# Kernel optimization log

Hardware: AMD Instinct MI355X
Metric: run time of the kernel (lower is better)

The kernel has to match this reference:

```python
import jax, jax.numpy as jnp
import numpy as np

B = 1024      # batch
D_NUM = 100   # numeric features
N_CAT = 20    # categorical features
CARD = 100    # cardinality per categorical feature
D = 1024      # d_token
DH = 675      # int(d_token * 0.66)
NT = D_NUM + 1 + N_CAT  # 121 tokens (CLS + numeric + categorical)
E = 4         # num_experts
K = 2         # top_k
MID = 512     # ResidualHead mid dim = max(D//2, 16)
RH = 256      # router/alpha hidden = max(D//4, 16)


def _ln(x, g, b):
    m = x.mean(-1, keepdims=True)
    v = ((x - m) ** 2).mean(-1, keepdims=True)
    return (x - m) * jax.lax.rsqrt(v + 1e-5) * g + b


def setup_inputs() -> dict:
    key = jax.random.key(0)
    ks = jax.random.split(key, 20)

    def n(i, shape, s=0.02):
        return jax.random.normal(ks[i], shape, dtype=jnp.float32) * s

    return dict(
        x_num=jax.random.normal(ks[0], (B, D_NUM), dtype=jnp.float32),
        x_cat=jax.random.randint(ks[1], (B, N_CAT), 0, CARD),
        tok_w=n(2, (D_NUM + 1, D), 0.05),
        tok_b=n(3, (D_NUM + N_CAT, D), 0.05),
        cat_emb=n(4, (N_CAT * CARD, D), 0.05),
        ln_g=jnp.ones((D,), jnp.float32), ln_b=jnp.zeros((D,), jnp.float32),
        lin0_w=n(5, (D, 2 * DH)), lin0_b=jnp.zeros((2 * DH,), jnp.float32),
        sgu_ln_g=jnp.ones((DH,), jnp.float32), sgu_ln_b=jnp.zeros((DH,), jnp.float32),
        sgu_w=n(6, (NT, NT), 0.05), sgu_b=jnp.zeros((NT,), jnp.float32),
        lin1_w=n(7, (DH, D)), lin1_b=jnp.zeros((D,), jnp.float32),
        r_w1=n(8, (D, RH)), r_b1=jnp.zeros((RH,), jnp.float32),
        r_w2=n(9, (RH, E)), r_b2=jnp.zeros((E,), jnp.float32),
        a_w1=n(10, (D, RH)), a_b1=jnp.zeros((RH,), jnp.float32),
        a_w2=n(11, (RH, 1)), a_b2=jnp.full((1,), -4.0, jnp.float32),
        base_w=n(12, (D, 1)), base_b=jnp.zeros((1,), jnp.float32),
        gh_w1=n(13, (D, MID), 0.001), gh_b1=jnp.zeros((MID,), jnp.float32),
        gh_w2=n(14, (MID, 1), 0.001), gh_b2=jnp.zeros((1,), jnp.float32),
        ex_w1=n(15, (E, D, MID), 0.001), ex_b1=jnp.zeros((E, MID), jnp.float32),
        ex_w2=n(16, (E, MID), 0.001), ex_b2=jnp.zeros((E,), jnp.float32),
    )


def reference(x_num, x_cat, tok_w, tok_b, cat_emb, ln_g, ln_b, lin0_w, lin0_b,
              sgu_ln_g, sgu_ln_b, sgu_w, sgu_b, lin1_w, lin1_b,
              r_w1, r_b1, r_w2, r_b2, a_w1, a_b1, a_w2, a_b2,
              base_w, base_b, gh_w1, gh_b1, gh_w2, gh_b2,
              ex_w1, ex_b1, ex_w2, ex_b2):
    # ---- Tokenizer ----
    offsets = jnp.arange(N_CAT) * CARD
    xn = jnp.concatenate([jnp.ones((x_num.shape[0], 1), x_num.dtype), x_num], axis=1)  # [B, D_NUM+1]
    x = tok_w[None] * xn[:, :, None]                                  # [B, D_NUM+1, D]
    x = jnp.concatenate([x, cat_emb[x_cat + offsets[None]]], axis=1)  # [B, NT, D]
    bias_full = jnp.concatenate([jnp.zeros((1, D), tok_b.dtype), tok_b], axis=0)
    x = x + bias_full[None]
    # ---- gMLP layer (n_layers=1) ----
    xr = x
    h = _ln(x, ln_g, ln_b)
    h = jax.nn.gelu(h @ lin0_w + lin0_b, approximate=False)           # [B, NT, 2*DH]
    u, v = h[..., :DH], h[..., DH:]
    v = _ln(v, sgu_ln_g, sgu_ln_b)
    # SGU token-mixing: out[b,s,d] = sum_t v[b,t,d] * W[s,t] + bias[s]
    v = jnp.einsum('btd,st->bsd', v, sgu_w) + sgu_b[None, :, None]
    x = (u * v) @ lin1_w + lin1_b
    x = x + xr
    # ---- pooled hidden (CLS token) ----
    hidden = jax.nn.gelu(_ln(x[:, 0], ln_g, ln_b), approximate=False)  # [B, D]
    # ---- router + top-k sparsification ----
    logits = jax.nn.relu(hidden @ r_w1 + r_b1) @ r_w2 + r_b2           # [B, E]
    dense = jax.nn.softmax(logits, axis=-1)
    vals, idx = jax.lax.top_k(dense, K)
    sparse = jnp.zeros_like(dense).at[jnp.arange(dense.shape[0])[:, None], idx].set(vals)
    rw = sparse / jnp.clip(sparse.sum(-1, keepdims=True), 1e-8)
    # ---- local experts (small residual heads, vectorized over E) ----
    eh = jax.nn.relu(jnp.einsum('bd,edm->bem', hidden, ex_w1) + ex_b1[None])
    eo = jnp.einsum('bem,em->be', eh, ex_w2) + ex_b2[None]             # [B, E]
    local = (rw * eo).sum(-1, keepdims=True)                           # [B, 1]
    # ---- global residual, alpha gate, base head ----
    glob = jax.nn.relu(hidden @ gh_w1 + gh_b1) @ gh_w2 + gh_b2
    alpha = jax.nn.sigmoid(jax.nn.relu(hidden @ a_w1 + a_b1) @ a_w2 + a_b2)
    y_base = hidden @ base_w + base_b
    return y_base + alpha * (glob + local)                             # [B, 1]
```

## Files before the change

kernel.cpp:

```cpp
#include <hip/hip_runtime.h>
#include <math.h>

#define B_SZ 1024

typedef __attribute__((ext_vector_type(8))) short bf16x8;
typedef __attribute__((ext_vector_type(4))) float f32x4;
typedef __attribute__((ext_vector_type(4))) float floatx4;
typedef __attribute__((ext_vector_type(4))) unsigned short ushortx4;

#define GLOAD16(src, dst) __builtin_amdgcn_global_load_lds( \
    (const __attribute__((address_space(1))) void*)(src), \
    (__attribute__((address_space(3))) void*)(dst), 16, 0, 0)

__device__ __forceinline__ unsigned short f2bf(float f) {
  unsigned int u = __float_as_uint(f);
  u += 0x7fff + ((u >> 16) & 1);
  return (unsigned short)(u >> 16);
}
__device__ __forceinline__ float bf2f(unsigned short b) {
  return __uint_as_float(((unsigned int)b) << 16);
}
__device__ __forceinline__ floatx4 b4f(ushortx4 u) {
  floatx4 r;
  r[0] = bf2f(u[0]); r[1] = bf2f(u[1]); r[2] = bf2f(u[2]); r[3] = bf2f(u[3]);
  return r;
}
__device__ __forceinline__ float gelu_exact(float x) {
  return 0.5f * x * (1.0f + erff(x * 0.70710678118654752f));
}
__device__ __forceinline__ float gelu_fast(float x) {
  const float c0 = 2.3022586f;
  const float c1 = 0.10295465f;
  float z = x * __builtin_fmaf(x * x, c1, c0);
  float e = __builtin_amdgcn_exp2f(z);
  float r = __builtin_amdgcn_rcpf(e + 1.0f);
  return __builtin_fmaf(-x, r, x);
}
__device__ __forceinline__ float wred(float v) {
#pragma unroll
  for (int o = 32; o > 0; o >>= 1) v += __shfl_xor(v, o, 64);
  return v;
}

struct PrepArgs {
  const float* src[9];
  unsigned short* dst[9];
  int ldin[9]; int coff[9]; int Nsrc[9]; int Ksrc[9]; int Kp[9];
  int nbx[9]; int blk0[10];
};

__global__ __launch_bounds__(256)
void prep_all(PrepArgs J,
              const float* __restrict__ tok_w, const float* __restrict__ tok_b,
              const float* __restrict__ cat_emb,
              const float* __restrict__ ln_g, const float* __restrict__ ln_b,
              const float* __restrict__ r_b1, const float* __restrict__ a_b1,
              const float* __restrict__ gh_b1, const float* __restrict__ ex_b1,
              unsigned short* __restrict__ Amat,
              float* __restrict__ nstat, float* __restrict__ cstat,
              float* __restrict__ bcat)
{
  const int bid = blockIdx.x;
  const int tid = threadIdx.x;
  const int lane = tid & 63;
  const int NT = J.blk0[9];
  if (bid < NT) {
    __shared__ float tile[64][65];
    int j = 0;
    while (bid >= J.blk0[j + 1]) ++j;
    const int bx = bid - J.blk0[j];
    const int k0 = (bx % J.nbx[j]) * 64;
    const int n0 = (bx / J.nbx[j]) * 64;
    const float* in = J.src[j];
    unsigned short* out = J.dst[j];
    const int ldin = J.ldin[j], coff = J.coff[j], Nsrc = J.Nsrc[j], Ksrc = J.Ksrc[j], Kp = J.Kp[j];
    const int kx = tid & 63;
    const int ry = tid >> 6;
    for (int r = ry; r < 64; r += 4) {
      const int k = k0 + r;
      const int n = n0 + kx;
      tile[r][kx] = (k < Ksrc && n < Nsrc) ? in[(size_t)k * ldin + coff + n] : 0.f;
    }
    __syncthreads();
    for (int r = ry; r < 64; r += 4) {
      const int n = n0 + r;
      const int k = k0 + kx;
      out[(size_t)n * Kp + k] = f2bf(tile[kx][r]);
    }
  } else if (bid < NT + 576) {
    const int r = (bid - NT) * 4 + (tid >> 6);
    if (r >= 2304) return;
    unsigned short* out = Amat + (size_t)r * 1024;
    for (int k = lane * 4; k < 1024; k += 256) {
      floatx4 g = *(const floatx4*)(ln_g + k);
      floatx4 v;
      if (r <= 100) {
        floatx4 a = *(const floatx4*)(tok_w + (size_t)r * 1024 + k);
#pragma unroll
        for (int q = 0; q < 4; q++) v[q] = a[q] * g[q];
      } else if (r <= 200) {
        floatx4 a = *(const floatx4*)(tok_b + (size_t)(r - 101) * 1024 + k);
#pragma unroll
        for (int q = 0; q < 4; q++) v[q] = a[q] * g[q];
      } else if (r <= 2200) {
        const int j = r - 201;
        const int c = j / 100;
        floatx4 a = *(const floatx4*)(cat_emb + (size_t)j * 1024 + k);
        floatx4 bq = *(const floatx4*)(tok_b + (size_t)(100 + c) * 1024 + k);
#pragma unroll
        for (int q = 0; q < 4; q++) v[q] = (a[q] + bq[q]) * g[q];
      } else if (r == 2201) {
        v = g;
      } else if (r == 2202) {
        v = *(const floatx4*)(ln_b + k);
      } else {
        v[0] = 0.f; v[1] = 0.f; v[2] = 0.f; v[3] = 0.f;
      }
      ushortx4 o;
#pragma unroll
      for (int q = 0; q < 4; q++) o[q] = f2bf(v[q]);
      *(ushortx4*)(out + k) = o;
    }
  } else if (bid < NT + 576 + 526) {
    const int w = (bid - NT - 576) * 4 + (tid >> 6);
    if (w >= 2101) return;
    if (w <= 100) {
      const int t = w;
      const float* wr = tok_w + (size_t)t * 1024;
      const float* br = (t >= 1) ? (tok_b + (size_t)(t - 1) * 1024) : nullptr;
      float sw = 0, sww = 0, sb = 0, sbb = 0, swb = 0;
      for (int k = lane * 4; k < 1024; k += 256) {
        floatx4 a = *(const floatx4*)(wr + k);
#pragma unroll
        for (int q = 0; q < 4; q++) { sw += a[q]; sww += a[q] * a[q]; }
        if (br) {
          floatx4 bq = *(const floatx4*)(br + k);
#pragma unroll
          for (int q = 0; q < 4; q++) { sb += bq[q]; sbb += bq[q] * bq[q]; swb += a[q] * bq[q]; }
        }
      }
      sw = wred(sw); sww = wred(sww); sb = wred(sb); sbb = wred(sbb); swb = wred(swb);
      if (lane == 0) {
        float* ns = nstat + (size_t)t * 5;
        ns[0] = sw; ns[1] = sww; ns[2] = sb; ns[3] = sbb; ns[4] = swb;
      }
    } else {
      const int j = w - 101;
      const int c = j / 100;
      const float* ar = cat_emb + (size_t)j * 1024;
      const float* br = tok_b + (size_t)(100 + c) * 1024;
      float s1 = 0, s2 = 0;
      for (int k = lane * 4; k < 1024; k += 256) {
        floatx4 a = *(const floatx4*)(ar + k);
        floatx4 bq = *(const floatx4*)(br + k);
#pragma unroll
        for (int q = 0; q < 4; q++) { const float v = a[q] + bq[q]; s1 += v; s2 += v * v; }
      }
      s1 = wred(s1); s2 = wred(s2);
      if (lane == 0) { cstat[(size_t)j * 2] = s1; cstat[(size_t)j * 2 + 1] = s2; }
    }
  } else {
    const int n = (bid - NT - 1102) * 256 + tid;
    if (n >= 3072) return;
    float v;
    if (n < 256) v = r_b1[n];
    else if (n < 512) v = a_b1[n - 256];
    else if (n < 1024) v = gh_b1[n - 512];
    else v = ex_b1[n - 1024];
    bcat[n] = v;
  }
}

template<int EPI>
__device__ __forceinline__
void gemm64_body(int bid, const unsigned short* __restrict__ A, long pitchA,
                 const unsigned short* __restrict__ Bw, int K,
                 const float* __restrict__ bias, const float* __restrict__ extra,
                 int NB, int Nvalid, int ldo,
                 float* __restrict__ outf, unsigned short* __restrict__ outb)
{
  __shared__ unsigned short As[64 * 32];
  __shared__ unsigned short Bs[64 * 32];
  const int tid = threadIdx.x, lane = tid & 63, wv = tid >> 6;
  const int nb = bid % NB, mb = bid / NB;
  const int m0 = mb * 64, n0 = nb * 64;
  const int wr = (wv >> 1) << 5, wc = (wv & 1) << 5;
  const int fr = lane & 15, fq = lane >> 4;

  const unsigned short* srcA = A + (size_t)(m0 + (tid >> 2)) * pitchA + ((tid & 3) << 3);
  const unsigned short* srcB = Bw + (size_t)(n0 + (tid >> 2)) * K + ((tid & 3) << 3);

  f32x4 acc[2][2] = {};
  for (int k0 = 0; k0 < K; k0 += 32) {
    __syncthreads();
    GLOAD16(srcA + k0, &As[tid * 8]);
    GLOAD16(srcB + k0, &Bs[tid * 8]);
    __syncthreads();
    bf16x8 af[2], bw_[2];
#pragma unroll
    for (int i = 0; i < 2; i++) {
      af[i]  = *(const bf16x8*)&As[(wr + i * 16 + fr) * 32 + fq * 8];
      bw_[i] = *(const bf16x8*)&Bs[(wc + i * 16 + fr) * 32 + fq * 8];
    }
#pragma unroll
    for (int i = 0; i < 2; i++)
#pragma unroll
      for (int j = 0; j < 2; j++)
        acc[i][j] = __builtin_amdgcn_mfma_f32_16x16x32_bf16(af[i], bw_[j], acc[i][j], 0, 0, 0);
  }

#pragma unroll
  for (int i = 0; i < 2; i++)
#pragma unroll
    for (int j = 0; j < 2; j++) {
      const int n = n0 + wc + j * 16 + fr;
      if (n >= ldo) continue;
      const bool valid = (n < Nvalid);
      const float bv = (EPI == 3 || EPI == 4) ? 0.f : (valid ? bias[n] : 0.f);
      const float ev = (EPI == 0) ? extra[n] : 0.f;
#pragma unroll
      for (int q = 0; q < 4; q++) {
        const int m = m0 + wr + i * 16 + fq * 4 + q;
        const float a = acc[i][j][q];
        if (EPI == 0) {
          outf[(size_t)m * ldo + n] = a + bv + ev;
        } else if (EPI == 1) {
          outb[(size_t)m * ldo + n] = f2bf(fmaxf(a + bv, 0.f));
        } else if (EPI == 3) {
          outf[(size_t)m * ldo + n] = a;
        } else {
          outb[(size_t)m * ldo + n] = f2bf(a);
        }
      }
    }
}

template<int EPI>
__global__ __launch_bounds__(256)
void gemm64(const unsigned short* __restrict__ A, long pitchA,
            const unsigned short* __restrict__ Bw, int K,
            const float* __restrict__ bias, const float* __restrict__ extra,
            int NB, int Nvalid, int ldo,
            float* __restrict__ outf, unsigned short* __restrict__ outb)
{
  gemm64_body<EPI>(blockIdx.x, A, pitchA, Bw, K, bias, extra, NB, Nvalid, ldo, outf, outb);
}

__device__ __forceinline__
void ucon_body(int bid, const float* __restrict__ lin0_w, const float* __restrict__ nstat,
               const float* __restrict__ tok_w, const float* __restrict__ ln_g,
               const float* __restrict__ ln_b, const float* __restrict__ lin0_b,
               float* __restrict__ ucon)
{
  __shared__ float xk[1024];
  __shared__ float part[4][64];
  const int tid = threadIdx.x;
  const float m = nstat[0] * (1.f / 1024.f);
  const float ex2 = nstat[1] * (1.f / 1024.f);
  const float rs = rsqrtf(ex2 - m * m + 1e-5f);
  for (int k = tid; k < 1024; k += 256)
    xk[k] = bf2f(f2bf((tok_w[k] - m) * rs * ln_g[k] + ln_b[k]));
  __syncthreads();
  const int c = bid * 64 + (tid & 63);
  const int ks = tid >> 6;
  float acc = 0.f;
  for (int k = ks * 256; k < ks * 256 + 256; k++)
    acc = __builtin_fmaf(xk[k], bf2f(f2bf(lin0_w[(size_t)k * 1350 + c])), acc);
  part[ks][tid & 63] = acc;
  __syncthreads();
  if (tid < 64) {
    const int cc = bid * 64 + tid;
    if (cc < 704) {
      const float s = part[0][tid] + part[1][tid] + part[2][tid] + part[3][tid];
      ucon[cc] = (cc < 675) ? gelu_exact(s + lin0_b[cc]) : 0.f;
    }
  }
}

__global__ __launch_bounds__(256)
void tab_and_u(const unsigned short* __restrict__ Amat, const unsigned short* __restrict__ w0v,
               unsigned short* __restrict__ TABb,
               const float* __restrict__ lin0_w, const float* __restrict__ nstat,
               const float* __restrict__ tok_w, const float* __restrict__ ln_g,
               const float* __restrict__ ln_b, const float* __restrict__ lin0_b,
               float* __restrict__ ucon)
{
  if (blockIdx.x < 432)
    gemm64_body<4>(blockIdx.x, Amat, 1024, w0v, 1024, nullptr, nullptr, 12, 768, 768, nullptr, TABb);
  else
    ucon_body(blockIdx.x - 432, lin0_w, nstat, tok_w, ln_g, ln_b, lin0_b, ucon);
}

__global__ __launch_bounds__(256)
void cat_rows(const unsigned short* __restrict__ TABb, const float* __restrict__ nstat,
              const float* __restrict__ cstat, const float* __restrict__ lin0_b,
              unsigned short* __restrict__ catvalb, float* __restrict__ catsc)
{
  const int r = blockIdx.x * 4 + (threadIdx.x >> 6);
  const int lane = threadIdx.x & 63;
  if (r >= 2001) return;
  float m, ex2;
  const unsigned short* T1;
  if (r < 2000) {
    m = cstat[(size_t)r * 2] * (1.f / 1024.f);
    ex2 = cstat[(size_t)r * 2 + 1] * (1.f / 1024.f);
    T1 = TABb + (size_t)(201 + r) * 768;
  } else {
    m = nstat[0] * (1.f / 1024.f);
    ex2 = nstat[1] * (1.f / 1024.f);
    T1 = TABb;
  }
  const float rs = rsqrtf(ex2 - m * m + 1e-5f);
  const float ga = -m * rs;
  const unsigned short* R = TABb + (size_t)2201 * 768;
  const unsigned short* C = TABb + (size_t)2202 * 768;
  const int dl = lane << 2;
  float s = 0.f, ss = 0.f;
  unsigned short* outp = catvalb + (size_t)r * 768;
#pragma unroll
  for (int ch = 0; ch < 3; ch++) {
    const int d = ch * 256 + dl;
    floatx4 t1 = b4f(*(const ushortx4*)(T1 + d));
    floatx4 rr = b4f(*(const ushortx4*)(R + d));
    floatx4 cc = b4f(*(const ushortx4*)(C + d));
    ushortx4 o;
#pragma unroll
    for (int q = 0; q < 4; q++) {
      const int dd = d + q;
      const float c2 = (dd < 675) ? (cc[q] + lin0_b[675 + dd]) : 0.f;
      const float pre = __builtin_fmaf(rs, t1[q], __builtin_fmaf(ga, rr[q], c2));
      const float g = (dd < 675) ? gelu_fast(pre) : 0.f;
      o[q] = f2bf(g); s += g; ss = __builtin_fmaf(g, g, ss);
    }
    *(ushortx4*)(outp + d) = o;
  }
  s = wred(s); ss = wred(ss);
  const float mu = s * (1.f / 675.f);
  const float rho = rsqrtf(ss * (1.f / 675.f) - mu * mu + 1e-5f);
  if (lane == 0) { catsc[(size_t)r * 2] = mu; catsc[(size_t)r * 2 + 1] = rho; }
}

__global__ __launch_bounds__(512)
void fused_v2(const unsigned short* __restrict__ TABb, const float* __restrict__ nstat,
              const float* __restrict__ catsc, const unsigned short* __restrict__ catvalb,
              const float* __restrict__ x_num, const int* __restrict__ x_cat,
              const float* __restrict__ sgu_ln_g, const float* __restrict__ sgu_ln_b,
              const float* __restrict__ sgu_w, const float* __restrict__ sgu_b,
              const float* __restrict__ lin0_b, const float* __restrict__ ucon,
              unsigned short* __restrict__ uv)
{
  const int b0 = blockIdx.x, b1 = blockIdx.x + 512;
  const int tid = threadIdx.x, lane = tid & 63, wv = tid >> 6;
  __shared__ float Rls[768], Cls[768];
  __shared__ float alf[2][100], bet[2][100], gam[2][100], swt[100];
  __shared__ float wrc[2][21], catkb[2][21];
  __shared__ int catrowS[2][21];
  __shared__ float accw[8][768];
  __shared__ float kbw[2][8];
  __shared__ float wss_s;

  for (int d = tid; d < 768; d += 512) {
    Rls[d] = (d < 675) ? bf2f(TABb[(size_t)2201 * 768 + d]) : 0.f;
    Cls[d] = (d < 675) ? (bf2f(TABb[(size_t)2202 * 768 + d]) + lin0_b[675 + d]) : 0.f;
  }
  if (tid < 200) {
    const int bb = tid / 100, tt = tid % 100;
    const int b = bb ? b1 : b0;
    const float sc = x_num[b * 100 + tt];
    const float* ns = nstat + (size_t)(tt + 1) * 5;
    const float m = (sc * ns[0] + ns[2]) * (1.f / 1024.f);
    const float ex2 = (sc * sc * ns[1] + 2.f * sc * ns[4] + ns[3]) * (1.f / 1024.f);
    const float rs = rsqrtf(ex2 - m * m + 1e-5f);
    alf[bb][tt] = rs * sc; bet[bb][tt] = rs; gam[bb][tt] = -m * rs;
    if (bb == 0) swt[tt] = sgu_w[tt + 1];
  } else if (tid < 242) {
    const int idx = tid - 200;
    const int bb = idx / 21, ii = idx % 21;
    const int b = bb ? b1 : b0;
    int row; float sw;
    if (ii < 20) { row = x_cat[b * 20 + ii] + 100 * ii; sw = sgu_w[101 + ii]; }
    else { row = 2000; sw = sgu_w[0]; }
    const float mu = catsc[(size_t)row * 2], rho = catsc[(size_t)row * 2 + 1];
    const float wr = sw * rho;
    wrc[bb][ii] = wr; catkb[bb][ii] = wr * mu; catrowS[bb][ii] = row;
  } else if (tid >= 256 && tid < 320) {
    float s = (lane < 121 ? sgu_w[lane] : 0.f) + (lane + 64 < 121 ? sgu_w[lane + 64] : 0.f);
    s = wred(s);
    if (lane == 0) wss_s = s;
  }
  __syncthreads();

  float accA[12] = {}, accB[12] = {};
  float kbA = 0.f, kbB = 0.f;
  const int dl = lane << 2;

  for (int i = 0; i < 13; i++) {
    const int tt = wv + 8 * i;
    if (tt >= 100) break;
    const float a0 = alf[0][tt], be0 = bet[0][tt], ga0 = gam[0][tt];
    const float a1 = alf[1][tt], be1 = bet[1][tt], ga1 = gam[1][tt];
    const unsigned short* T1 = TABb + (size_t)(tt + 1) * 768;
    const unsigned short* T2 = TABb + (size_t)(101 + tt) * 768;
    float s0 = 0.f, ss0 = 0.f, s1 = 0.f, ss1 = 0.f;
    float va[12], vb[12];
#pragma unroll
    for (int ch = 0; ch < 3; ch++) {
      const int d = ch * 256 + dl;
      floatx4 t1 = b4f(*(const ushortx4*)(T1 + d));
      floatx4 t2 = b4f(*(const ushortx4*)(T2 + d));
      floatx4 rr = *(const floatx4*)(&Rls[d]);
      floatx4 cc = *(const floatx4*)(&Cls[d]);
#pragma unroll
      for (int q = 0; q < 4; q++) {
        const float pre0 = __builtin_fmaf(a0, t1[q], __builtin_fmaf(be0, t2[q], __builtin_fmaf(ga0, rr[q], cc[q])));
        const float g0 = gelu_fast(pre0);
        va[ch * 4 + q] = g0; s0 += g0; ss0 = __builtin_fmaf(g0, g0, ss0);
        const float pre1 = __builtin_fmaf(a1, t1[q], __builtin_fmaf(be1, t2[q], __builtin_fmaf(ga1, rr[q], cc[q])));
        const float g1 = gelu_fast(pre1);
        vb[ch * 4 + q] = g1; s1 += g1; ss1 = __builtin_fmaf(g1, g1, ss1);
      }
    }
    s0 = wred(s0); ss0 = wred(ss0); s1 = wred(s1); ss1 = wred(ss1);
    const float sw = swt[tt];
    const float mu0 = s0 * (1.f / 675.f);
    const float rho0 = rsqrtf(ss0 * (1.f / 675.f) - mu0 * mu0 + 1e-5f);
    const float w0 = sw * rho0;
    const float mu1 = s1 * (1.f / 675.f);
    const float rho1 = rsqrtf(ss1 * (1.f / 675.f) - mu1 * mu1 + 1e-5f);
    const float w1 = sw * rho1;
#pragma unroll
    for (int q = 0; q < 12; q++) {
      accA[q] = __builtin_fmaf(w0, va[q], accA[q]);
      accB[q] = __builtin_fmaf(w1, vb[q], accB[q]);
    }
    kbA = __builtin_fmaf(w0, mu0, kbA);
    kbB = __builtin_fmaf(w1, mu1, kbB);
  }

  for (int i = 0; i < 3; i++) {
    const int ii = wv + 8 * i;
    if (ii >= 21) break;
    {
      const float wr = wrc[0][ii];
      const unsigned short* cv = catvalb + (size_t)catrowS[0][ii] * 768;
#pragma unroll
      for (int ch = 0; ch < 3; ch++) {
        floatx4 v = b4f(*(const ushortx4*)(cv + ch * 256 + dl));
#pragma unroll
        for (int q = 0; q < 4; q++) accA[ch * 4 + q] = __builtin_fmaf(wr, v[q], accA[ch * 4 + q]);
      }
    }
    {
      const float wr = wrc[1][ii];
      const unsigned short* cv = catvalb + (size_t)catrowS[1][ii] * 768;
#pragma unroll
      for (int ch = 0; ch < 3; ch++) {
        floatx4 v = b4f(*(const ushortx4*)(cv + ch * 256 + dl));
#pragma unroll
        for (int q = 0; q < 4; q++) accB[ch * 4 + q] = __builtin_fmaf(wr, v[q], accB[ch * 4 + q]);
      }
    }
  }
  if (lane == 0) { kbw[0][wv] = kbA; kbw[1][wv] = kbB; }

  const float sb0 = sgu_b[0];

#pragma unroll
  for (int ch = 0; ch < 3; ch++)
    *(floatx4*)&accw[wv][ch * 256 + dl] = *(const floatx4*)&accA[ch * 4];
  __syncthreads();
  {
    float kbs = 0.f;
#pragma unroll
    for (int w = 0; w < 8; w++) kbs += kbw[0][w];
#pragma unroll
    for (int i = 0; i < 21; i++) kbs += catkb[0][i];
    const float wss = wss_s;
    for (int d = tid; d < 704; d += 512) {
      unsigned short o = 0;
      if (d < 675) {
        float a = 0.f;
#pragma unroll
        for (int w = 0; w < 8; w++) a += accw[w][d];
        const float v0 = sgu_ln_g[d] * (a - kbs) + sgu_ln_b[d] * wss + sb0;
        o = f2bf(ucon[d] * v0);
      }
      uv[(size_t)b0 * 704 + d] = o;
    }
  }
  __syncthreads();
#pragma unroll
  for (int ch = 0; ch < 3; ch++)
    *(floatx4*)&accw[wv][ch * 256 + dl] = *(const floatx4*)&accB[ch * 4];
  __syncthreads();
  {
    float kbs = 0.f;
#pragma unroll
    for (int w = 0; w < 8; w++) kbs += kbw[1][w];
#pragma unroll
    for (int i = 0; i < 21; i++) kbs += catkb[1][i];
    const float wss = wss_s;
    for (int d = tid; d < 704; d += 512) {
      unsigned short o = 0;
      if (d < 675) {
        float a = 0.f;
#pragma unroll
        for (int w = 0; w < 8; w++) a += accw[w][d];
        const float v0 = sgu_ln_g[d] * (a - kbs) + sgu_ln_b[d] * wss + sb0;
        o = f2bf(ucon[d] * v0);
      }
      uv[(size_t)b1 * 704 + d] = o;
    }
  }
}

__global__ __launch_bounds__(256)
void ln_gelu_hidden(const float* __restrict__ xfin,
                    const float* __restrict__ ln_g, const float* __restrict__ ln_b,
                    const float* __restrict__ base_w,
                    unsigned short* __restrict__ hid_bf, float* __restrict__ base_y)
{
  const int w = (blockIdx.x * 256 + threadIdx.x) >> 6;
  const int lane = threadIdx.x & 63;
  if (w >= B_SZ) return;
  const float* row = xfin + (size_t)w * 1024;
  float s = 0.f, ss = 0.f;
  for (int k = lane; k < 1024; k += 64) { float v = row[k]; s += v; ss += v * v; }
  s = wred(s); ss = wred(ss);
  const float m = s * (1.f / 1024.f);
  const float var = ss * (1.f / 1024.f) - m * m;
  const float rs = rsqrtf(var + 1e-5f);
  float bacc = 0.f;
  for (int k = lane; k < 1024; k += 64) {
    float v = gelu_fast((row[k] - m) * rs * ln_g[k] + ln_b[k]);
    hid_bf[(size_t)w * 1024 + k] = f2bf(v);
    bacc = __builtin_fmaf(v, base_w[k], bacc);
  }
  bacc = wred(bacc);
  if (lane == 0) base_y[w] = bacc;
}

__global__ __launch_bounds__(256)
void final_head(const unsigned short* __restrict__ H1, const float* __restrict__ base_y,
                const float* __restrict__ r_w2, const float* __restrict__ r_b2,
                const float* __restrict__ a_w2, const float* __restrict__ a_b2,
                const float* __restrict__ gh_w2, const float* __restrict__ gh_b2,
                const float* __restrict__ ex_w2, const float* __restrict__ ex_b2,
                const float* __restrict__ base_b,
                float* __restrict__ out)
{
  const int b = blockIdx.x;
  const int tid = threadIdx.x;
  const unsigned short* h1 = H1 + (size_t)b * 3072;
  float p[10];
#pragma unroll
  for (int i = 0; i < 10; i++) p[i] = 0.f;
  {
    const int m = tid;
    const float hr = bf2f(h1[m]);
    p[0] = hr * r_w2[m * 4 + 0];
    p[1] = hr * r_w2[m * 4 + 1];
    p[2] = hr * r_w2[m * 4 + 2];
    p[3] = hr * r_w2[m * 4 + 3];
    const float ha = bf2f(h1[256 + m]);
    p[4] = ha * a_w2[m];
  }
  for (int m = tid; m < 512; m += 256) {
    p[5] += bf2f(h1[512 + m]) * gh_w2[m];
#pragma unroll
    for (int e = 0; e < 4; e++)
      p[6 + e] += bf2f(h1[1024 + e * 512 + m]) * ex_w2[e * 512 + m];
  }

  __shared__ float red[10][4];
  const int lane = tid & 63, wv = tid >> 6;
#pragma unroll
  for (int i = 0; i < 10; i++) {
    const float v = wred(p[i]);
    if (lane == 0) red[i][wv] = v;
  }
  __syncthreads();
  if (tid == 0) {
    float s[10];
#pragma unroll
    for (int i = 0; i < 10; i++) s[i] = red[i][0] + red[i][1] + red[i][2] + red[i][3];
    float lg[4];
#pragma unroll
    for (int e = 0; e < 4; e++) lg[e] = s[e] + r_b2[e];
    const float mx = fmaxf(fmaxf(lg[0], lg[1]), fmaxf(lg[2], lg[3]));
    float den[4]; float dsum = 0.f;
#pragma unroll
    for (int e = 0; e < 4; e++) { den[e] = expf(lg[e] - mx); dsum += den[e]; }
#pragma unroll
    for (int e = 0; e < 4; e++) den[e] /= dsum;
    int i1 = 0;
    for (int e = 1; e < 4; e++) if (den[e] > den[i1]) i1 = e;
    int i2 = -1;
    for (int e = 0; e < 4; e++) { if (e == i1) continue; if (i2 < 0 || den[e] > den[i2]) i2 = e; }
    float eo[4];
#pragma unroll
    for (int e = 0; e < 4; e++) eo[e] = s[6 + e] + ex_b2[e];
    const float v1 = den[i1], v2 = den[i2];
    const float ssum = fmaxf(v1 + v2, 1e-8f);
    const float local = (v1 * eo[i1] + v2 * eo[i2]) / ssum;
    const float glob = s[5] + gh_b2[0];
    const float alpha = 1.0f / (1.0f + expf(-(s[4] + a_b2[0])));
    out[b] = base_y[b] + base_b[0] + alpha * (glob + local);
  }
}

extern "C" void kernel_launch(void* const* d_in, const int* in_sizes, int n_in,
                              void* d_out, int out_size, void* d_ws, size_t ws_size,
                              hipStream_t stream)
{
  const float* x_num  = (const float*)d_in[0];
  const int*   x_cat  = (const int*)d_in[1];
  const float* tok_w  = (const float*)d_in[2];
  const float* tok_b  = (const float*)d_in[3];
  const float* cat_emb= (const float*)d_in[4];
  const float* ln_g   = (const float*)d_in[5];
  const float* ln_b   = (const float*)d_in[6];
  const float* lin0_w = (const float*)d_in[7];
  const float* lin0_b = (const float*)d_in[8];
  const float* sgu_ln_g = (const float*)d_in[9];
  const float* sgu_ln_b = (const float*)d_in[10];
  const float* sgu_w  = (const float*)d_in[11];
  const float* sgu_b  = (const float*)d_in[12];
  const float* lin1_w = (const float*)d_in[13];
  const float* lin1_b = (const float*)d_in[14];
  const float* r_w1   = (const float*)d_in[15];
  const float* r_b1   = (const float*)d_in[16];
  const float* r_w2   = (const float*)d_in[17];
  const float* r_b2   = (const float*)d_in[18];
  const float* a_w1   = (const float*)d_in[19];
  const float* a_b1   = (const float*)d_in[20];
  const float* a_w2   = (const float*)d_in[21];
  const float* a_b2   = (const float*)d_in[22];
  const float* base_w = (const float*)d_in[23];
  const float* base_b = (const float*)d_in[24];
  const float* gh_w1  = (const float*)d_in[25];
  const float* gh_b1  = (const float*)d_in[26];
  const float* gh_w2  = (const float*)d_in[27];
  const float* gh_b2  = (const float*)d_in[28];
  const float* ex_w1  = (const float*)d_in[29];
  const float* ex_b1  = (const float*)d_in[30];
  const float* ex_w2  = (const float*)d_in[31];
  const float* ex_b2  = (const float*)d_in[32];
  (void)in_sizes; (void)n_in; (void)out_size; (void)ws_size;

  char* ws = (char*)d_ws;
  size_t off = 0;
  auto alloc = [&](size_t bytes) { void* p = ws + off; off += (bytes + 255) & ~(size_t)255; return p; };

  unsigned short* w0v  = (unsigned short*)alloc((size_t)768 * 1024 * 2);
  unsigned short* w1t  = (unsigned short*)alloc((size_t)1024 * 704 * 2);
  unsigned short* wcat = (unsigned short*)alloc((size_t)3072 * 1024 * 2);
  float* bcat          = (float*)alloc((size_t)3072 * 4);
  unsigned short* Amat = (unsigned short*)alloc((size_t)2304 * 1024 * 2);
  unsigned short* TABb = (unsigned short*)alloc((size_t)2304 * 768 * 2);
  float* nstat         = (float*)alloc((size_t)101 * 5 * 4);
  float* cstat         = (float*)alloc((size_t)2000 * 2 * 4);
  unsigned short* catvalb = (unsigned short*)alloc((size_t)2001 * 768 * 2);
  float* catsc         = (float*)alloc((size_t)2001 * 2 * 4);
  float* ucon          = (float*)alloc((size_t)704 * 4);
  unsigned short* uv   = (unsigned short*)alloc((size_t)B_SZ * 704 * 2);
  float* xfin          = (float*)alloc((size_t)B_SZ * 1024 * 4);
  float* base_y        = (float*)alloc((size_t)B_SZ * 4);
  unsigned short* hidb = (unsigned short*)alloc((size_t)B_SZ * 1024 * 2);
  unsigned short* H1   = (unsigned short*)alloc((size_t)B_SZ * 3072 * 2);

  const dim3 blk(256);

  PrepArgs J;
  auto setJ = [&](int i, const float* s, unsigned short* d, int ldin, int coff,
                  int Nsrc, int Ksrc, int Kp, int nbx, int nby) {
    J.src[i] = s; J.dst[i] = d; J.ldin[i] = ldin; J.coff[i] = coff;
    J.Nsrc[i] = Nsrc; J.Ksrc[i] = Ksrc; J.Kp[i] = Kp; J.nbx[i] = nbx;
    J.blk0[i + 1] = J.blk0[i] + nbx * nby;
  };
  J.blk0[0] = 0;
  setJ(0, lin0_w, w0v, 1350, 675, 675, 1024, 1024, 16, 12);
  setJ(1, lin1_w, w1t, 1024, 0,  1024,  675,  704, 11, 16);
  setJ(2, r_w1,  wcat,                          256, 0, 256, 1024, 1024, 16, 4);
  setJ(3, a_w1,  wcat + (size_t)256 * 1024,     256, 0, 256, 1024, 1024, 16, 4);
  setJ(4, gh_w1, wcat + (size_t)512 * 1024,     512, 0, 512, 1024, 1024, 16, 8);
  for (int e = 0; e < 4; e++)
    setJ(5 + e, ex_w1 + (size_t)e * 1024 * 512,
         wcat + (size_t)(1024 + e * 512) * 1024, 512, 0, 512, 1024, 1024, 16, 8);

  const int nprep = J.blk0[9] + 576 + 526 + 12;
  prep_all<<<nprep, blk, 0, stream>>>(J, tok_w, tok_b, cat_emb, ln_g, ln_b,
      r_b1, a_b1, gh_b1, ex_b1, Amat, nstat, cstat, bcat);

  tab_and_u<<<443, blk, 0, stream>>>(Amat, w0v, TABb, lin0_w, nstat, tok_w, ln_g, ln_b, lin0_b, ucon);

  cat_rows<<<501, blk, 0, stream>>>(TABb, nstat, cstat, lin0_b, catvalb, catsc);

  fused_v2<<<512, dim3(512), 0, stream>>>(TABb, nstat, catsc, catvalb, x_num, x_cat,
      sgu_ln_g, sgu_ln_b, sgu_w, sgu_b, lin0_b, ucon, uv);

  gemm64<0><<<16 * 16, blk, 0, stream>>>(uv, 704, w1t, 704,
      lin1_b, tok_w, 16, 1024, 1024, xfin, nullptr);
  ln_gelu_hidden<<<B_SZ / 4, blk, 0, stream>>>(xfin, ln_g, ln_b, base_w, hidb, base_y);
  gemm64<1><<<16 * 48, blk, 0, stream>>>(hidb, 1024, wcat, 1024,
      bcat, nullptr, 48, 3072, 3072, nullptr, H1);

  final_head<<<B_SZ, blk, 0, stream>>>(H1, base_y, r_w2, r_b2, a_w2, a_b2, gh_w2, gh_b2,
                                       ex_w2, ex_b2, base_b, (float*)d_out);
}
```

Measured before the change: 140.3 us.

## Fuse second-layer head projections into the hidden GEMM epilogue via atomics

The head GEMM no longer writes the bf16 H1 activation matrix. Its epilogue now applies ReLU, multiplies by the second-layer weights, reduces each row through LDS atomics, and adds the per-row partial sums into a small global buffer with global atomics. The buffer is zeroed by extra blocks in the prep kernel. A tiny per-batch-row kernel replaces final_head and does the softmax/top-k/gate maths, removing the H1 write/read round trip. In exchange it adds LDS and global atomic contention and a nondeterministic summation order.

```diff
diff --git a/kernel.cpp b/kernel.cpp
--- a/kernel.cpp
+++ b/kernel.cpp
@@ -58,7 +58,7 @@
               const float* __restrict__ gh_b1, const float* __restrict__ ex_b1,
               unsigned short* __restrict__ Amat,
               float* __restrict__ nstat, float* __restrict__ cstat,
-              float* __restrict__ bcat)
+              float* __restrict__ bcat, float* __restrict__ sums)
 {
   const int bid = blockIdx.x;
   const int tid = threadIdx.x;
@@ -159,7 +159,7 @@
       s1 = wred(s1); s2 = wred(s2);
       if (lane == 0) { cstat[(size_t)j * 2] = s1; cstat[(size_t)j * 2 + 1] = s2; }
     }
-  } else {
+  } else if (bid < NT + 576 + 526 + 12) {
     const int n = (bid - NT - 1102) * 256 + tid;
     if (n >= 3072) return;
     float v;
@@ -168,6 +168,9 @@
     else if (n < 1024) v = gh_b1[n - 512];
     else v = ex_b1[n - 1024];
     bcat[n] = v;
+  } else {
+    const int idx = (bid - NT - 1114) * 256 + tid;
+    if (idx < B_SZ * 10) sums[idx] = 0.f;
   }
 }
 
@@ -244,6 +247,94 @@
             float* __restrict__ outf, unsigned short* __restrict__ outb)
 {
   gemm64_body<EPI>(blockIdx.x, A, pitchA, Bw, K, bias, extra, NB, Nvalid, ldo, outf, outb);
+}
+
+__global__ __launch_bounds__(256)
+void gemm_heads(const unsigned short* __restrict__ A,
+                const unsigned short* __restrict__ Bw,
+                const float* __restrict__ bias,
+                const float* __restrict__ r_w2, const float* __restrict__ a_w2,
+                const float* __restrict__ gh_w2, const float* __restrict__ ex_w2,
+                float* __restrict__ sums)
+{
+  __shared__ unsigned short As[64 * 32];
+  __shared__ unsigned short Bs[64 * 32];
+  __shared__ float hacc[64][4];
+  const int K = 1024, NB = 48;
+  const int tid = threadIdx.x, lane = tid & 63, wv = tid >> 6;
+  const int bid = blockIdx.x;
+  const int nb = bid % NB, mb = bid / NB;
+  const int m0 = mb * 64, n0 = nb * 64;
+  const int wr = (wv >> 1) << 5, wc = (wv & 1) << 5;
+  const int fr = lane & 15, fq = lane >> 4;
+
+  hacc[tid >> 2][tid & 3] = 0.f;
+
+  const unsigned short* srcA = A + (size_t)(m0 + (tid >> 2)) * K + ((tid & 3) << 3);
+  const unsigned short* srcB = Bw + (size_t)(n0 + (tid >> 2)) * K + ((tid & 3) << 3);
+
+  f32x4 acc[2][2] = {};
+  for (int k0 = 0; k0 < K; k0 += 32) {
+    __syncthreads();
+    GLOAD16(srcA + k0, &As[tid * 8]);
+    GLOAD16(srcB + k0, &Bs[tid * 8]);
+    __syncthreads();
+    bf16x8 af[2], bw_[2];
+#pragma unroll
+    for (int i = 0; i < 2; i++) {
+      af[i]  = *(const bf16x8*)&As[(wr + i * 16 + fr) * 32 + fq * 8];
+      bw_[i] = *(const bf16x8*)&Bs[(wc + i * 16 + fr) * 32 + fq * 8];
+    }
+#pragma unroll
+    for (int i = 0; i < 2; i++)
+#pragma unroll
+      for (int j = 0; j < 2; j++)
+        acc[i][j] = __builtin_amdgcn_mfma_f32_16x16x32_bf16(af[i], bw_[j], acc[i][j], 0, 0, 0);
+  }
+  __syncthreads();
+
+  const int region = (nb < 4) ? 0 : (nb < 8) ? 1 : (nb < 16) ? 2 : 3;
+#pragma unroll
+  for (int i = 0; i < 2; i++)
+#pragma unroll
+    for (int j = 0; j < 2; j++) {
+      const int n = n0 + wc + j * 16 + fr;
+      const float bv = bias[n];
+      float w0 = 0.f, w1 = 0.f, w2 = 0.f, w3 = 0.f;
+      if (region == 0) {
+        w0 = r_w2[n * 4 + 0]; w1 = r_w2[n * 4 + 1];
+        w2 = r_w2[n * 4 + 2]; w3 = r_w2[n * 4 + 3];
+      } else if (region == 1) {
+        w0 = a_w2[n - 256];
+      } else if (region == 2) {
+        w0 = gh_w2[n - 512];
+      } else {
+        w0 = ex_w2[n - 1024];
+      }
+#pragma unroll
+      for (int q = 0; q < 4; q++) {
+        const int ml = wr + i * 16 + fq * 4 + q;
+        const float val = fmaxf(acc[i][j][q] + bv, 0.f);
+        atomicAdd(&hacc[ml][0], val * w0);
+        if (region == 0) {
+          atomicAdd(&hacc[ml][1], val * w1);
+          atomicAdd(&hacc[ml][2], val * w2);
+          atomicAdd(&hacc[ml][3], val * w3);
+        }
+      }
+    }
+  __syncthreads();
+
+  if (region == 0) {
+    if (tid < 256) {
+      const int row = tid >> 2, e = tid & 3;
+      atomicAdd(&sums[(size_t)(m0 + row) * 10 + e], hacc[row][e]);
+    }
+  } else {
+    const int slot = (region == 1) ? 4 : (region == 2) ? 5 : (6 + (nb - 16) / 8);
+    if (tid < 64)
+      atomicAdd(&sums[(size_t)(m0 + tid) * 10 + slot], hacc[tid][0]);
+  }
 }
 
 __device__ __forceinline__
@@ -541,72 +632,37 @@
 }
 
 __global__ __launch_bounds__(256)
-void final_head(const unsigned short* __restrict__ H1, const float* __restrict__ base_y,
-                const float* __restrict__ r_w2, const float* __restrict__ r_b2,
-                const float* __restrict__ a_w2, const float* __restrict__ a_b2,
-                const float* __restrict__ gh_w2, const float* __restrict__ gh_b2,
-                const float* __restrict__ ex_w2, const float* __restrict__ ex_b2,
-                const float* __restrict__ base_b,
-                float* __restrict__ out)
-{
-  const int b = blockIdx.x;
-  const int tid = threadIdx.x;
-  const unsigned short* h1 = H1 + (size_t)b * 3072;
-  float p[10];
-#pragma unroll
-  for (int i = 0; i < 10; i++) p[i] = 0.f;
-  {
-    const int m = tid;
-    const float hr = bf2f(h1[m]);
-    p[0] = hr * r_w2[m * 4 + 0];
-    p[1] = hr * r_w2[m * 4 + 1];
-    p[2] = hr * r_w2[m * 4 + 2];
-    p[3] = hr * r_w2[m * 4 + 3];
-    const float ha = bf2f(h1[256 + m]);
-    p[4] = ha * a_w2[m];
-  }
-  for (int m = tid; m < 512; m += 256) {
-    p[5] += bf2f(h1[512 + m]) * gh_w2[m];
-#pragma unroll
-    for (int e = 0; e < 4; e++)
-      p[6 + e] += bf2f(h1[1024 + e * 512 + m]) * ex_w2[e * 512 + m];
-  }
-
-  __shared__ float red[10][4];
-  const int lane = tid & 63, wv = tid >> 6;
-#pragma unroll
-  for (int i = 0; i < 10; i++) {
-    const float v = wred(p[i]);
-    if (lane == 0) red[i][wv] = v;
-  }
-  __syncthreads();
-  if (tid == 0) {
-    float s[10];
-#pragma unroll
-    for (int i = 0; i < 10; i++) s[i] = red[i][0] + red[i][1] + red[i][2] + red[i][3];
-    float lg[4];
-#pragma unroll
-    for (int e = 0; e < 4; e++) lg[e] = s[e] + r_b2[e];
-    const float mx = fmaxf(fmaxf(lg[0], lg[1]), fmaxf(lg[2], lg[3]));
-    float den[4]; float dsum = 0.f;
-#pragma unroll
-    for (int e = 0; e < 4; e++) { den[e] = expf(lg[e] - mx); dsum += den[e]; }
-#pragma unroll
-    for (int e = 0; e < 4; e++) den[e] /= dsum;
-    int i1 = 0;
-    for (int e = 1; e < 4; e++) if (den[e] > den[i1]) i1 = e;
-    int i2 = -1;
-    for (int e = 0; e < 4; e++) { if (e == i1) continue; if (i2 < 0 || den[e] > den[i2]) i2 = e; }
-    float eo[4];
-#pragma unroll
-    for (int e = 0; e < 4; e++) eo[e] = s[6 + e] + ex_b2[e];
-    const float v1 = den[i1], v2 = den[i2];
-    const float ssum = fmaxf(v1 + v2, 1e-8f);
-    const float local = (v1 * eo[i1] + v2 * eo[i2]) / ssum;
-    const float glob = s[5] + gh_b2[0];
-    const float alpha = 1.0f / (1.0f + expf(-(s[4] + a_b2[0])));
-    out[b] = base_y[b] + base_b[0] + alpha * (glob + local);
-  }
+void final_small(const float* __restrict__ sums, const float* __restrict__ base_y,
+                 const float* __restrict__ r_b2, const float* __restrict__ a_b2,
+                 const float* __restrict__ gh_b2, const float* __restrict__ ex_b2,
+                 const float* __restrict__ base_b,
+                 float* __restrict__ out)
+{
+  const int b = blockIdx.x * 256 + threadIdx.x;
+  if (b >= B_SZ) return;
+  const float* s = sums + (size_t)b * 10;
+  float lg[4];
+#pragma unroll
+  for (int e = 0; e < 4; e++) lg[e] = s[e] + r_b2[e];
+  const float mx = fmaxf(fmaxf(lg[0], lg[1]), fmaxf(lg[2], lg[3]));
+  float den[4]; float dsum = 0.f;
+#pragma unroll
+  for (int e = 0; e < 4; e++) { den[e] = expf(lg[e] - mx); dsum += den[e]; }
+#pragma unroll
+  for (int e = 0; e < 4; e++) den[e] /= dsum;
+  int i1 = 0;
+  for (int e = 1; e < 4; e++) if (den[e] > den[i1]) i1 = e;
+  int i2 = -1;
+  for (int e = 0; e < 4; e++) { if (e == i1) continue; if (i2 < 0 || den[e] > den[i2]) i2 = e; }
+  float eo[4];
+#pragma unroll
+  for (int e = 0; e < 4; e++) eo[e] = s[6 + e] + ex_b2[e];
+  const float v1 = den[i1], v2 = den[i2];
+  const float ssum = fmaxf(v1 + v2, 1e-8f);
+  const float local = (v1 * eo[i1] + v2 * eo[i2]) / ssum;
+  const float glob = s[5] + gh_b2[0];
+  const float alpha = 1.0f / (1.0f + expf(-(s[4] + a_b2[0])));
+  out[b] = base_y[b] + base_b[0] + alpha * (glob + local);
 }
 
 extern "C" void kernel_launch(void* const* d_in, const int* in_sizes, int n_in,
@@ -667,7 +723,7 @@
   float* xfin          = (float*)alloc((size_t)B_SZ * 1024 * 4);
   float* base_y        = (float*)alloc((size_t)B_SZ * 4);
   unsigned short* hidb = (unsigned short*)alloc((size_t)B_SZ * 1024 * 2);
-  unsigned short* H1   = (unsigned short*)alloc((size_t)B_SZ * 3072 * 2);
+  float* sums          = (float*)alloc((size_t)B_SZ * 10 * 4);
 
   const dim3 blk(256);
 
@@ -688,9 +744,9 @@
     setJ(5 + e, ex_w1 + (size_t)e * 1024 * 512,
          wcat + (size_t)(1024 + e * 512) * 1024, 512, 0, 512, 1024, 1024, 16, 8);
 
-  const int nprep = J.blk0[9] + 576 + 526 + 12;
+  const int nprep = J.blk0[9] + 576 + 526 + 12 + 40;
   prep_all<<<nprep, blk, 0, stream>>>(J, tok_w, tok_b, cat_emb, ln_g, ln_b,
-      r_b1, a_b1, gh_b1, ex_b1, Amat, nstat, cstat, bcat);
+      r_b1, a_b1, gh_b1, ex_b1, Amat, nstat, cstat, bcat, sums);
 
   tab_and_u<<<443, blk, 0, stream>>>(Amat, w0v, TABb, lin0_w, nstat, tok_w, ln_g, ln_b, lin0_b, ucon);
 
@@ -702,9 +758,7 @@
   gemm64<0><<<16 * 16, blk, 0, stream>>>(uv, 704, w1t, 704,
       lin1_b, tok_w, 16, 1024, 1024, xfin, nullptr);
   ln_gelu_hidden<<<B_SZ / 4, blk, 0, stream>>>(xfin, ln_g, ln_b, base_w, hidb, base_y);
-  gemm64<1><<<16 * 48, blk, 0, stream>>>(hidb, 1024, wcat, 1024,
-      bcat, nullptr, 48, 3072, 3072, nullptr, H1);
-
-  final_head<<<B_SZ, blk, 0, stream>>>(H1, base_y, r_w2, r_b2, a_w2, a_b2, gh_w2, gh_b2,
-                                       ex_w2, ex_b2, base_b, (float*)d_out);
-}
+  gemm_heads<<<16 * 48, blk, 0, stream>>>(hidb, wcat, bcat, r_w2, a_w2, gh_w2, ex_w2, sums);
+
+  final_small<<<4, blk, 0, stream>>>(sums, base_y, r_b2, a_b2, gh_b2, ex_b2, base_b, (float*)d_out);
+}
```

New measurement: 173.7 us. 1.24x slower.
